# Kernel optimization log

Hardware: AMD Instinct MI355X
Metric: run time of the kernel (lower is better)

## Reference

```python
import jax, jax.numpy as jnp
import numpy as np

B, L, D = 4, 4096, 1024
DS, EXP, DC = 16, 2, 4
DI = EXP * D
K_SYM = max(3, 2 * DC + 1)  # 9


def _linear(x, w, b):
    # torch nn.Linear: y = x @ W^T + b, W:[out,in]
    return jnp.einsum('blc,oc->blo', x, w) + b


def _dwconv(x, kernel, bias, pad_l, pad_r):
    # x:[B,L,C], kernel:[C,1,k] depthwise, torch 'same' padding (asymmetric for even k)
    y = jax.lax.conv_general_dilated(
        x.transpose(0, 2, 1), kernel, window_strides=(1,),
        padding=[(pad_l, pad_r)], dimension_numbers=('NCH', 'OIH', 'NCH'),
        feature_group_count=x.shape[-1])
    return y.transpose(0, 2, 1) + bias


def _rmsnorm(x, w, eps=1e-6):
    scale = jax.lax.rsqrt(jnp.mean(x * x, axis=-1, keepdims=True) + eps)
    return w * x * scale


def setup_inputs() -> dict:
    key = jax.random.key(0)
    ks = jax.random.split(key, 12)
    def n(k, shape, s=0.02):
        return jax.random.normal(k, shape, jnp.float32) * s
    return {
        'x': jax.random.normal(ks[0], (B, L, D), jnp.float32),
        'norm_w': jnp.ones((D,), jnp.float32),
        'in_w': n(ks[1], (2 * DI, D)), 'in_b': jnp.zeros((2 * DI,), jnp.float32),
        'dwa_k': n(ks[2], (DI, 1, DC)), 'dwa_b': jnp.zeros((DI,), jnp.float32),
        'A': n(ks[3], (DI, DS)), 'Bm': n(ks[4], (DS, DI)),
        'sym_k': n(ks[5], (DI, 1, K_SYM)), 'sym_b': jnp.zeros((DI,), jnp.float32),
        'pw_w': n(ks[6], (DI, DI)), 'pw_b': jnp.zeros((DI,), jnp.float32),
        'ha_w': n(ks[7], (DI // 2, DI)), 'ha_b': jnp.zeros((DI // 2,), jnp.float32),
        'hb_w': n(ks[8], (DI // 2, DI)), 'hb_b': jnp.zeros((DI // 2,), jnp.float32),
        'fuse_w': n(ks[9], (DI, DI)), 'fuse_b': jnp.zeros((DI,), jnp.float32),
        'out_w': n(ks[10], (D, DI)), 'out_b': jnp.zeros((D,), jnp.float32),
    }


def reference(x, norm_w, in_w, in_b, dwa_k, dwa_b, A, Bm, sym_k, sym_b,
              pw_w, pw_b, ha_w, ha_b, hb_w, hb_b, fuse_w, fuse_b, out_w, out_b):
    residual = x
    h = _rmsnorm(x, norm_w)
    h = _linear(h, in_w, in_b)                       # [B,L,2*DI]
    gate, val = h[..., :DI], h[..., DI:]
    gate = jax.nn.sigmoid(gate)
    # mamba-like branch: depthwise conv (k=4, torch 'same' -> pad (1,2)) + low-rank A@B
    a = _dwconv(val, dwa_k, dwa_b, 1, 2)             # [B,L,DI]
    a = jnp.einsum('bld,ds->bls', a, A)              # [B,L,DS]
    a = jnp.einsum('bls,sd->bld', a, Bm)             # [B,L,DI]
    # symmetric conv branch: depthwise conv (k=9, pad (4,4)) -> silu -> pointwise linear
    b = _dwconv(val, sym_k, sym_b, K_SYM // 2, K_SYM // 2)
    b = jax.nn.silu(b)
    b = _linear(b, pw_w, pw_b)
    a = _linear(a, ha_w, ha_b)                       # [B,L,DI/2]
    b = _linear(b, hb_w, hb_b)                       # [B,L,DI/2]
    y = jnp.concatenate([a, b], axis=-1)             # [B,L,DI]
    y = _linear(y, fuse_w, fuse_b)
    y = gate * y
    y = _linear(y, out_w, out_b)                     # [B,L,D]
    return residual + y
```

## Files before the change

### kernel.cpp

```cpp
#include <hip/hip_runtime.h>
#include <hip/hip_bf16.h>
#include <stdint.h>

typedef __bf16 bf16;
typedef __bf16 bf16x8 __attribute__((ext_vector_type(8)));
typedef __bf16 bf16x4 __attribute__((ext_vector_type(4)));
typedef float  f32x4  __attribute__((ext_vector_type(4)));

#define LDS_PTR(p) ((__attribute__((address_space(3))) uint32_t*)(p))
#define GLB_PTR(p) ((const __attribute__((address_space(1))) uint32_t*)(p))

static constexpr int BATCH = 4, SEQ = 4096, DMODEL = 1024;
static constexpr int DI = 2048;
static constexpr int MTOK = BATCH * SEQ;

enum { EPI_SPLIT = 0, EPI_PLAIN = 1, EPI_GATE = 2, EPI_RES = 3, EPI_F32S = 4 };

template <int EPI, bool SPLITK = false, bool KEXT = false>
__global__ __launch_bounds__(256) void gemm_bt(
    const bf16* __restrict__ Aact, const bf16* __restrict__ W,
    const float* __restrict__ bias,
    bf16* __restrict__ out0, bf16* __restrict__ out1,
    const bf16* __restrict__ gate,
    float* __restrict__ outf, const float* __restrict__ resid,
    int N, int K, int ldC, int col_off,
    const bf16* __restrict__ Ax, const bf16* __restrict__ Bx)
{
  __shared__ __align__(16) bf16 sA[128 * 64];
  __shared__ __align__(16) bf16 sB[128 * 64];
  const int tid  = threadIdx.x;
  int n0, m0, kbeg, kend;
  size_t out_off = 0;
  if (SPLITK) {
    n0 = blockIdx.z * 128;
    m0 = blockIdx.y * 128;
    const int kh = K / gridDim.x;
    kbeg = blockIdx.x * kh; kend = kbeg + kh;
    out_off = (EPI == EPI_F32S) ? (size_t)blockIdx.x * (size_t)col_off
                                : (size_t)blockIdx.x * ((size_t)MTOK * 128);
  } else {
    const int nT  = gridDim.x;
    const int lin = blockIdx.y * nT + blockIdx.x;
    const int grp = lin / (8 * nT);
    const int within = lin - grp * (8 * nT);
    n0 = (within >> 3) * 128;
    m0 = (grp * 8 + (within & 7)) * 128;
    kbeg = 0; kend = K;
  }
  const int lane = tid & 63;
  const int wv   = tid >> 6;
  const int wr   = wv >> 1, wc = wv & 1;
  const int l15  = lane & 15, quad = lane >> 4;

  f32x4 acc[4][4];
#pragma unroll
  for (int i = 0; i < 4; ++i)
#pragma unroll
    for (int j = 0; j < 4; ++j) acc[i][j] = (f32x4){0.f, 0.f, 0.f, 0.f};

  int rr[4], cb[4];
#pragma unroll
  for (int j = 0; j < 4; ++j) {
    const int s = tid + j * 256;
    rr[j] = s >> 3;
    cb[j] = ((s & 7) ^ (rr[j] & 7)) * 16;
  }

  const char* gA = (const char*)(Aact + (size_t)m0 * K);
  const char* gW = (const char*)(W + (size_t)n0 * K);

  const int ntile = (kend - kbeg) >> 6;
  const int ttot  = KEXT ? ntile + 1 : ntile;
  for (int ti = 0; ti < ttot; ++ti) {
    if (ti) __syncthreads();
    if (!KEXT || ti < ntile) {
      const int k0 = kbeg + ti * 64;
#pragma unroll
      for (int j = 0; j < 4; ++j)
        __builtin_amdgcn_global_load_lds(GLB_PTR(gA + ((size_t)rr[j] * K + k0) * 2 + cb[j]),
                                         LDS_PTR(sA + (tid + j * 256) * 8), 16, 0, 0);
#pragma unroll
      for (int j = 0; j < 4; ++j)
        __builtin_amdgcn_global_load_lds(GLB_PTR(gW + ((size_t)rr[j] * K + k0) * 2 + cb[j]),
                                         LDS_PTR(sB + (tid + j * 256) * 8), 16, 0, 0);
    } else {
#pragma unroll
      for (int j = 0; j < 4; ++j)
        __builtin_amdgcn_global_load_lds(GLB_PTR((const char*)Ax + ((size_t)(m0 + rr[j]) * 64) * 2 + cb[j]),
                                         LDS_PTR(sA + (tid + j * 256) * 8), 16, 0, 0);
#pragma unroll
      for (int j = 0; j < 4; ++j)
        __builtin_amdgcn_global_load_lds(GLB_PTR((const char*)Bx + ((size_t)(n0 + rr[j]) * 64) * 2 + cb[j]),
                                         LDS_PTR(sB + (tid + j * 256) * 8), 16, 0, 0);
    }
    __syncthreads();

#pragma unroll
    for (int h = 0; h < 2; ++h) {
      bf16x8 av[4], bv[4];
#pragma unroll
      for (int t = 0; t < 4; ++t) {
        const int Ra = wr * 64 + t * 16 + l15;
        const int Rb = wc * 64 + t * 16 + l15;
        const int cc = h * 4 + quad;
        av[t] = *(const bf16x8*)(sA + (Ra * 8 + (cc ^ (Ra & 7))) * 8);
        bv[t] = *(const bf16x8*)(sB + (Rb * 8 + (cc ^ (Rb & 7))) * 8);
      }
#pragma unroll
      for (int i = 0; i < 4; ++i)
#pragma unroll
        for (int j = 0; j < 4; ++j)
          acc[i][j] = __builtin_amdgcn_mfma_f32_16x16x32_bf16(av[i], bv[j], acc[i][j], 0, 0, 0);
    }
  }

  bf16*  o0 = out0 + out_off;
  float* of = outf ? outf + out_off : nullptr;
#pragma unroll
  for (int i = 0; i < 4; ++i) {
    const int mbase = m0 + wr * 64 + i * 16 + quad * 4;
#pragma unroll
    for (int j = 0; j < 4; ++j) {
      const int n = n0 + wc * 64 + j * 16 + l15;
      const float bj = bias ? bias[n] : 0.f;
#pragma unroll
      for (int r = 0; r < 4; ++r) {
        const int mm = mbase + r;
        float v = acc[i][j][r] + bj;
        if (EPI == EPI_SPLIT) {
          if (n < DI) o0[(size_t)mm * DI + n] = (bf16)(1.f / (1.f + __expf(-v)));
          else        out1[(size_t)mm * DI + (n - DI)] = (bf16)v;
        } else if (EPI == EPI_PLAIN) {
          o0[(size_t)mm * ldC + col_off + n] = (bf16)v;
        } else if (EPI == EPI_GATE) {
          const float g = (float)gate[(size_t)mm * DI + n];
          o0[(size_t)mm * ldC + n] = (bf16)(v * g);
        } else if (EPI == EPI_F32S) {
          of[(size_t)mm * ldC + n] = v;
        } else {
          outf[(size_t)mm * ldC + n] = v + resid[(size_t)mm * ldC + n];
        }
      }
    }
  }
}

__global__ __launch_bounds__(256) void rmsnorm_kernel(
    const float* __restrict__ x, const float* __restrict__ w, bf16* __restrict__ out)
{
  const int row = blockIdx.x;
  const int tid = threadIdx.x;
  const float4 xv = ((const float4*)(x + (size_t)row * DMODEL))[tid];
  float s = xv.x * xv.x + xv.y * xv.y + xv.z * xv.z + xv.w * xv.w;
#pragma unroll
  for (int o = 32; o; o >>= 1) s += __shfl_xor(s, o);
  __shared__ float red[4];
  if ((tid & 63) == 0) red[tid >> 6] = s;
  __syncthreads();
  const float tot = red[0] + red[1] + red[2] + red[3];
  const float scale = rsqrtf(tot * (1.f / DMODEL) + 1e-6f);
  const float4 wv = ((const float4*)w)[tid];
  bf16x4 o4 = { (bf16)(xv.x * wv.x * scale), (bf16)(xv.y * wv.y * scale),
                (bf16)(xv.z * wv.z * scale), (bf16)(xv.w * wv.w * scale) };
  *(bf16x4*)(out + (size_t)row * DMODEL + tid * 4) = o4;
}

static constexpr int TL2 = 32;
__global__ __launch_bounds__(256) void conv_kernel(
    const bf16* __restrict__ val,
    const float* __restrict__ sym_k, const float* __restrict__ sym_b,
    bf16* __restrict__ bbuf)
{
  const int d  = (blockIdx.y * 256 + threadIdx.x) * 4;
  const int b  = blockIdx.z;
  const int l0 = blockIdx.x * TL2;
  float wk[9][4], bs[4];
#pragma unroll
  for (int j = 0; j < 4; ++j) {
    bs[j] = sym_b[d + j];
#pragma unroll
    for (int k = 0; k < 9; ++k) wk[k][j] = sym_k[(d + j) * 9 + k];
  }
  const bf16* base = val + (size_t)b * SEQ * DI + d;

  float win[9][4];
#pragma unroll
  for (int j = 0; j < 8; ++j) {
    const int xr = l0 + j - 4;
    if (xr >= 0 && xr < SEQ) {
      bf16x4 v = *(const bf16x4*)(base + (size_t)xr * DI);
#pragma unroll
      for (int c = 0; c < 4; ++c) win[j][c] = (float)v[c];
    } else {
#pragma unroll
      for (int c = 0; c < 4; ++c) win[j][c] = 0.f;
    }
  }
  for (int t = 0; t < TL2; ++t) {
    const int xf = l0 + t + 4;
    if (xf < SEQ) {
      bf16x4 v = *(const bf16x4*)(base + (size_t)xf * DI);
#pragma unroll
      for (int c = 0; c < 4; ++c) win[8][c] = (float)v[c];
    } else {
#pragma unroll
      for (int c = 0; c < 4; ++c) win[8][c] = 0.f;
    }
    float sb[4];
#pragma unroll
    for (int c = 0; c < 4; ++c) sb[c] = bs[c];
#pragma unroll
    for (int k = 0; k < 9; ++k)
#pragma unroll
      for (int c = 0; c < 4; ++c) sb[c] += win[k][c] * wk[k][c];
    bf16x4 o;
#pragma unroll
    for (int c = 0; c < 4; ++c) o[c] = (bf16)(sb[c] / (1.f + __expf(-sb[c])));
    *(bf16x4*)(bbuf + ((size_t)b * SEQ + l0 + t) * DI + d) = o;
#pragma unroll
    for (int k = 0; k < 8; ++k)
#pragma unroll
      for (int c = 0; c < 4; ++c) win[k][c] = win[k + 1][c];
  }
}

__global__ __launch_bounds__(256) void prep_cvt_kernel(
    const float* __restrict__ in_w, const float* __restrict__ hb_w,
    const float* __restrict__ out_w, const float* __restrict__ pw_w,
    bf16* __restrict__ in_wbf, bf16* __restrict__ hb_bf,
    bf16* __restrict__ out_bf, bf16* __restrict__ pwT_bf)
{
  __shared__ float s[32][33];
  const int b = blockIdx.x;
  const int tid = threadIdx.x;
  if (b < 8192) {
    const float* src; bf16* dst; size_t i;
    if (b < 4096)      { src = in_w;  dst = in_wbf; i = (size_t)b * 256 + tid; }
    else if (b < 6144) { src = hb_w;  dst = hb_bf;  i = (size_t)(b - 4096) * 256 + tid; }
    else               { src = out_w; dst = out_bf; i = (size_t)(b - 6144) * 256 + tid; }
    const float4 v = ((const float4*)src)[i];
    bf16x4 o4 = { (bf16)v.x, (bf16)v.y, (bf16)v.z, (bf16)v.w };
    *(bf16x4*)(dst + 4 * i) = o4;
  } else {
    const int q = b - 8192;
    const int d0 = (q & 63) * 32, c0 = (q >> 6) * 32;
    const int r = tid >> 5, x = tid & 31;
#pragma unroll
    for (int rr = r; rr < 32; rr += 8)
      s[rr][x] = pw_w[(size_t)(c0 + rr) * 2048 + d0 + x];
    __syncthreads();
#pragma unroll
    for (int rr = r; rr < 32; rr += 8)
      pwT_bf[(size_t)(d0 + rr) * 2048 + c0 + x] = (bf16)s[x][rr];
  }
}

__global__ __launch_bounds__(256) void prep_small_kernel(
    const float* __restrict__ Bm, const float* __restrict__ ha_w,
    const float* __restrict__ dwa_b, const float* __restrict__ dwa_k,
    const float* __restrict__ A,
    const float* __restrict__ hb_w, const float* __restrict__ pw_b,
    const float* __restrict__ hb_b, const float* __restrict__ fuse_w,
    const float* __restrict__ Hp,
    float* __restrict__ T1, float* __restrict__ cvec, float* __restrict__ b_H,
    bf16* __restrict__ Wp, bf16* __restrict__ Fb, bf16* __restrict__ Ht)
{
  const int b = blockIdx.x, tid = threadIdx.x;
  __shared__ float red[4][16];
  if (b < 1024) {
    const int o = b;
    float acc[16];
#pragma unroll
    for (int s = 0; s < 16; ++s) acc[s] = 0.f;
    for (int d = tid; d < 2048; d += 256) {
      const float w = ha_w[(size_t)o * 2048 + d];
#pragma unroll
      for (int s = 0; s < 16; ++s) acc[s] += Bm[s * 2048 + d] * w;
    }
    const int lane = tid & 63, wv = tid >> 6;
#pragma unroll
    for (int s = 0; s < 16; ++s) {
      float v = acc[s];
#pragma unroll
      for (int off = 32; off; off >>= 1) v += __shfl_xor(v, off);
      if (lane == s) red[wv][s] = v;
    }
    __syncthreads();
    if (tid < 16)
      T1[tid * 1024 + o] = red[0][tid] + red[1][tid] + red[2][tid] + red[3][tid];
  } else if (b == 1024) {
    float acc[16];
#pragma unroll
    for (int s = 0; s < 16; ++s) acc[s] = 0.f;
    for (int d = tid; d < 2048; d += 256) {
      const float w = dwa_b[d];
#pragma unroll
      for (int s = 0; s < 16; ++s) acc[s] += w * A[d * 16 + s];
    }
    const int lane = tid & 63, wv = tid >> 6;
#pragma unroll
    for (int s = 0; s < 16; ++s) {
      float v = acc[s];
#pragma unroll
      for (int off = 32; off; off >>= 1) v += __shfl_xor(v, off);
      if (lane == s) red[wv][s] = v;
    }
    __syncthreads();
    if (tid < 16) cvec[tid] = red[0][tid] + red[1][tid] + red[2][tid] + red[3][tid];
  } else if (b < 1029) {
    const int o = (b - 1025) * 256 + tid;
    float acc = hb_b[o];
    const float* hr = hb_w + (size_t)o * 2048;
    for (int c = 0; c < 2048; c += 4) {
      float4 h = *(const float4*)(hr + c);
      float4 p = *(const float4*)(pw_b + c);
      acc += h.x * p.x + h.y * p.y + h.z * p.z + h.w * p.w;
    }
    b_H[o] = acc;
  } else if (b < 1037) {
    const int d = (b - 1029) * 256 + tid;
    float kk[4], av[16];
#pragma unroll
    for (int k = 0; k < 4; ++k) kk[k] = dwa_k[d * 4 + k];
#pragma unroll
    for (int s = 0; s < 16; ++s) av[s] = A[d * 16 + s];
#pragma unroll
    for (int k = 0; k < 4; ++k)
#pragma unroll
      for (int s = 0; s < 16; ++s)
        Wp[(size_t)(k * 16 + s) * 2048 + d] = (bf16)(kk[k] * av[s]);
    for (int n = 64; n < 128; ++n) Wp[(size_t)n * 2048 + d] = (bf16)0.f;
  } else if (b < 3085) {
    const int idx = (b - 1037) * 256 + tid;
    const int n = idx >> 8, o4 = idx & 255;
    float4 v = ((const float4*)(fuse_w + (size_t)n * 2048 + 1024))[o4];
    bf16x4 o = { (bf16)v.x, (bf16)v.y, (bf16)v.z, (bf16)v.w };
    *(bf16x4*)(Fb + (size_t)n * 1024 + o4 * 4) = o;
  } else {
    const size_t e4 = (size_t)(b - 3085) * 256 + tid;
    float4 p0 = ((const float4*)Hp)[e4];
    float4 p1 = ((const float4*)(Hp + 2048 * 1024))[e4];
    bf16x4 o = { (bf16)(p0.x + p1.x), (bf16)(p0.y + p1.y),
                 (bf16)(p0.z + p1.z), (bf16)(p0.w + p1.w) };
    *(bf16x4*)(Ht + e4 * 4) = o;
  }
}

__global__ __launch_bounds__(256) void prep_fuse_kernel(
    const float* __restrict__ T1, const float* __restrict__ fuse_w,
    const float* __restrict__ fuse_b, const float* __restrict__ ha_b,
    const float* __restrict__ b_H,
    bf16* __restrict__ T2e, float* __restrict__ bias_z)
{
  const int b = blockIdx.x, tid = threadIdx.x;
  if (b < 128) {
    const int n = b * 16 + (tid >> 4);
    const int s = tid & 15;
    const float* fr = fuse_w + (size_t)n * 2048;
    const float* tr = T1 + s * 1024;
    float acc = 0.f;
    for (int o = 0; o < 1024; o += 4) {
      float4 f = *(const float4*)(fr + o);
      float4 t = *(const float4*)(tr + o);
      acc += f.x * t.x + f.y * t.y + f.z * t.z + f.w * t.w;
    }
    T2e[(size_t)n * 64 + s]      = (bf16)acc;
    T2e[(size_t)n * 64 + s + 16] = (bf16)0.f;
    T2e[(size_t)n * 64 + s + 32] = (bf16)0.f;
    T2e[(size_t)n * 64 + s + 48] = (bf16)0.f;
  } else {
    const int n = b - 128;
    const float* fr = fuse_w + (size_t)n * 2048;
    const int o = tid * 4;
    float4 fa = *(const float4*)(fr + o);
    float4 fb = *(const float4*)(fr + 1024 + o);
    float4 ha = *(const float4*)(ha_b + o);
    float4 bh = *(const float4*)(b_H + o);
    float acc = fa.x * ha.x + fa.y * ha.y + fa.z * ha.z + fa.w * ha.w
              + fb.x * bh.x + fb.y * bh.y + fb.z * bh.z + fb.w * bh.w;
#pragma unroll
    for (int off = 32; off; off >>= 1) acc += __shfl_xor(acc, off);
    __shared__ float r4[4];
    if ((tid & 63) == 0) r4[tid >> 6] = acc;
    __syncthreads();
    if (tid == 0) bias_z[n] = fuse_b[n] + r4[0] + r4[1] + r4[2] + r4[3];
  }
}

__global__ __launch_bounds__(256) void s16_kernel(
    const bf16* __restrict__ P0, const bf16* __restrict__ P1,
    const float* __restrict__ cvec, bf16* __restrict__ s16e)
{
  const int g = blockIdx.x * 256 + threadIdx.x;
  const int tok = g >> 4, s = g & 15;
  const int l = tok & (SEQ - 1), bb = tok >> 12;
  float acc = cvec[s];
#pragma unroll
  for (int k = 0; k < 4; ++k) {
    const int r = l - 1 + k;
    if ((unsigned)r < (unsigned)SEQ) {
      const size_t idx = ((size_t)bb * SEQ + r) * 128 + k * 16 + s;
      acc += (float)P0[idx] + (float)P1[idx];
    }
  }
  s16e[(size_t)tok * 64 + s]      = (bf16)acc;
  s16e[(size_t)tok * 64 + s + 16] = (bf16)0.f;
  s16e[(size_t)tok * 64 + s + 32] = (bf16)0.f;
  s16e[(size_t)tok * 64 + s + 48] = (bf16)0.f;
}

extern "C" void kernel_launch(void* const* d_in, const int* in_sizes, int n_in,
                              void* d_out, int out_size, void* d_ws, size_t ws_size,
                              hipStream_t stream)
{
  const float* x      = (const float*)d_in[0];
  const float* norm_w = (const float*)d_in[1];
  const float* in_w   = (const float*)d_in[2];
  const float* in_b   = (const float*)d_in[3];
  const float* dwa_k  = (const float*)d_in[4];
  const float* dwa_b  = (const float*)d_in[5];
  const float* Amat   = (const float*)d_in[6];
  const float* Bm     = (const float*)d_in[7];
  const float* sym_k  = (const float*)d_in[8];
  const float* sym_b  = (const float*)d_in[9];
  const float* pw_w   = (const float*)d_in[10];
  const float* pw_b   = (const float*)d_in[11];
  const float* ha_w   = (const float*)d_in[12];
  const float* ha_b   = (const float*)d_in[13];
  const float* hb_w   = (const float*)d_in[14];
  const float* hb_b   = (const float*)d_in[15];
  const float* fuse_w = (const float*)d_in[16];
  const float* fuse_b = (const float*)d_in[17];
  const float* out_w  = (const float*)d_in[18];
  const float* out_b  = (const float*)d_in[19];
  float* out = (float*)d_out;

  char* ws = (char*)d_ws;
  const size_t MB = 1u << 20, KB = 1u << 10;
  bf16*  in_wbf  = (bf16*)(ws + 0);
  bf16*  hnorm   = (bf16*)(ws + 8 * MB);
  bf16*  bsilu   = (bf16*)(ws + 0);
  float* Hpart   = (float*)(ws + 64 * MB);
  bf16*  valp    = (bf16*)(ws + 64 * MB);
  bf16*  zbuf    = (bf16*)(ws + 64 * MB);
  bf16*  gatep   = (bf16*)(ws + 128 * MB);
  bf16*  Pbuf    = (bf16*)(ws + 192 * MB);
  bf16*  pwT_bf  = (bf16*)(ws + 200 * MB);
  bf16*  WB_bf   = (bf16*)(ws + 200 * MB);
  bf16*  hb_bf   = (bf16*)(ws + 208 * MB);
  bf16*  Fb_bf   = (bf16*)(ws + 208 * MB);
  bf16*  s16e    = (bf16*)(ws + 208 * MB);
  bf16*  Ht_bf   = (bf16*)(ws + 212 * MB);
  bf16*  out_bf  = (bf16*)(ws + 216 * MB);
  float* T1      = (float*)(ws + 220 * MB);
  float* cvec    = (float*)(ws + 220 * MB + 64 * KB);
  float* b_H     = (float*)(ws + 220 * MB + 68 * KB);
  float* bias_z  = (float*)(ws + 220 * MB + 72 * KB);
  bf16*  Wp      = (bf16*)(ws + 220 * MB + 80 * KB);
  bf16*  T2e     = (bf16*)(ws + 220 * MB + 592 * KB);

  prep_cvt_kernel<<<12288, 256, 0, stream>>>(
      in_w, hb_w, out_w, pw_w, in_wbf, hb_bf, out_bf, pwT_bf);
  gemm_bt<EPI_F32S, true><<<dim3(2, 16, 8), 256, 0, stream>>>(
      pwT_bf, hb_bf, nullptr, nullptr, nullptr, nullptr, Hpart, nullptr,
      1024, 2048, 1024, 2048 * 1024, nullptr, nullptr);
  prep_small_kernel<<<5133, 256, 0, stream>>>(
      Bm, ha_w, dwa_b, dwa_k, Amat, hb_w, pw_b, hb_b, fuse_w, Hpart,
      T1, cvec, b_H, Wp, Fb_bf, Ht_bf);
  gemm_bt<EPI_PLAIN><<<dim3(16, 16), 256, 0, stream>>>(
      Fb_bf, Ht_bf, nullptr, WB_bf, nullptr, nullptr, nullptr, nullptr,
      2048, 1024, 2048, 0, nullptr, nullptr);
  prep_fuse_kernel<<<2176, 256, 0, stream>>>(T1, fuse_w, fuse_b, ha_b, b_H, T2e, bias_z);

  rmsnorm_kernel<<<MTOK, 256, 0, stream>>>(x, norm_w, hnorm);
  gemm_bt<EPI_SPLIT><<<dim3(32, 128), 256, 0, stream>>>(
      hnorm, in_wbf, in_b, gatep, valp, nullptr, nullptr, nullptr,
      4096, 1024, DI, 0, nullptr, nullptr);
  conv_kernel<<<dim3(SEQ / TL2, 2, BATCH), 256, 0, stream>>>(
      valp, sym_k, sym_b, bsilu);
  gemm_bt<EPI_PLAIN, true><<<dim3(2, 128), 256, 0, stream>>>(
      valp, Wp, nullptr, Pbuf, nullptr, nullptr, nullptr, nullptr,
      128, 2048, 128, 0, nullptr, nullptr);
  s16_kernel<<<MTOK * 16 / 256, 256, 0, stream>>>(
      Pbuf, Pbuf + (size_t)MTOK * 128, cvec, s16e);
  gemm_bt<EPI_GATE, false, true><<<dim3(16, 128), 256, 0, stream>>>(
      bsilu, WB_bf, bias_z, zbuf, nullptr, gatep, nullptr, nullptr,
      2048, 2048, 2048, 0, s16e, T2e);
  gemm_bt<EPI_RES><<<dim3(8, 128), 256, 0, stream>>>(
      zbuf, out_bf, out_b, nullptr, nullptr, nullptr, out, x,
      1024, 2048, 1024, 0, nullptr, nullptr);
}
```

Measured before the change: 836.7 us.

## Restructure weight-prep pipeline with wider split-K and merged prep kernels

Merges the small precompute work into the first conversion kernel so it runs concurrently with the bf16 weight casts. The Ht split-K GEMM grid is widened (8 K-partitions reduced by a new combine kernel), and the WB GEMM becomes split-K with fp32 partials reduced inside prep_fuse. The T2e dot products are spread over four threads each with shuffle reductions. The aim is to fill the GPU during the small weight-preprocessing GEMMs, at the cost of extra fp32 partial traffic and one added launch.

Result: faster. 806.3 us (-3.6%).

```diff
diff --git a/kernel.cpp b/kernel.cpp
--- a/kernel.cpp
+++ b/kernel.cpp
@@ -224,15 +224,21 @@
   }
 }
 
-__global__ __launch_bounds__(256) void prep_cvt_kernel(
+__global__ __launch_bounds__(256) void prep1_kernel(
     const float* __restrict__ in_w, const float* __restrict__ hb_w,
     const float* __restrict__ out_w, const float* __restrict__ pw_w,
+    const float* __restrict__ Bm, const float* __restrict__ ha_w,
+    const float* __restrict__ dwa_b, const float* __restrict__ dwa_k,
+    const float* __restrict__ A, const float* __restrict__ pw_b,
+    const float* __restrict__ hb_b, const float* __restrict__ fuse_w,
     bf16* __restrict__ in_wbf, bf16* __restrict__ hb_bf,
-    bf16* __restrict__ out_bf, bf16* __restrict__ pwT_bf)
+    bf16* __restrict__ out_bf, bf16* __restrict__ pwT_bf,
+    float* __restrict__ T1, float* __restrict__ cvec, float* __restrict__ b_H,
+    bf16* __restrict__ Wp, bf16* __restrict__ Fb)
 {
   __shared__ float s[32][33];
-  const int b = blockIdx.x;
-  const int tid = threadIdx.x;
+  __shared__ float red[4][16];
+  const int b = blockIdx.x, tid = threadIdx.x;
   if (b < 8192) {
     const float* src; bf16* dst; size_t i;
     if (b < 4096)      { src = in_w;  dst = in_wbf; i = (size_t)b * 256 + tid; }
@@ -241,7 +247,7 @@
     const float4 v = ((const float4*)src)[i];
     bf16x4 o4 = { (bf16)v.x, (bf16)v.y, (bf16)v.z, (bf16)v.w };
     *(bf16x4*)(dst + 4 * i) = o4;
-  } else {
+  } else if (b < 12288) {
     const int q = b - 8192;
     const int d0 = (q & 63) * 32, c0 = (q >> 6) * 32;
     const int r = tid >> 5, x = tid & 31;
@@ -252,63 +258,48 @@
 #pragma unroll
     for (int rr = r; rr < 32; rr += 8)
       pwT_bf[(size_t)(d0 + rr) * 2048 + c0 + x] = (bf16)s[x][rr];
-  }
-}
-
-__global__ __launch_bounds__(256) void prep_small_kernel(
-    const float* __restrict__ Bm, const float* __restrict__ ha_w,
-    const float* __restrict__ dwa_b, const float* __restrict__ dwa_k,
-    const float* __restrict__ A,
-    const float* __restrict__ hb_w, const float* __restrict__ pw_b,
-    const float* __restrict__ hb_b, const float* __restrict__ fuse_w,
-    const float* __restrict__ Hp,
-    float* __restrict__ T1, float* __restrict__ cvec, float* __restrict__ b_H,
-    bf16* __restrict__ Wp, bf16* __restrict__ Fb, bf16* __restrict__ Ht)
-{
-  const int b = blockIdx.x, tid = threadIdx.x;
-  __shared__ float red[4][16];
-  if (b < 1024) {
-    const int o = b;
+  } else if (b < 13312) {
+    const int o = b - 12288;
     float acc[16];
 #pragma unroll
-    for (int s = 0; s < 16; ++s) acc[s] = 0.f;
+    for (int ss = 0; ss < 16; ++ss) acc[ss] = 0.f;
     for (int d = tid; d < 2048; d += 256) {
       const float w = ha_w[(size_t)o * 2048 + d];
 #pragma unroll
-      for (int s = 0; s < 16; ++s) acc[s] += Bm[s * 2048 + d] * w;
+      for (int ss = 0; ss < 16; ++ss) acc[ss] += Bm[ss * 2048 + d] * w;
     }
     const int lane = tid & 63, wv = tid >> 6;
 #pragma unroll
-    for (int s = 0; s < 16; ++s) {
-      float v = acc[s];
+    for (int ss = 0; ss < 16; ++ss) {
+      float v = acc[ss];
 #pragma unroll
       for (int off = 32; off; off >>= 1) v += __shfl_xor(v, off);
-      if (lane == s) red[wv][s] = v;
+      if (lane == ss) red[wv][ss] = v;
     }
     __syncthreads();
     if (tid < 16)
       T1[tid * 1024 + o] = red[0][tid] + red[1][tid] + red[2][tid] + red[3][tid];
-  } else if (b == 1024) {
+  } else if (b == 13312) {
     float acc[16];
 #pragma unroll
-    for (int s = 0; s < 16; ++s) acc[s] = 0.f;
+    for (int ss = 0; ss < 16; ++ss) acc[ss] = 0.f;
     for (int d = tid; d < 2048; d += 256) {
       const float w = dwa_b[d];
 #pragma unroll
-      for (int s = 0; s < 16; ++s) acc[s] += w * A[d * 16 + s];
+      for (int ss = 0; ss < 16; ++ss) acc[ss] += w * A[d * 16 + ss];
     }
     const int lane = tid & 63, wv = tid >> 6;
 #pragma unroll
-    for (int s = 0; s < 16; ++s) {
-      float v = acc[s];
+    for (int ss = 0; ss < 16; ++ss) {
+      float v = acc[ss];
 #pragma unroll
       for (int off = 32; off; off >>= 1) v += __shfl_xor(v, off);
-      if (lane == s) red[wv][s] = v;
+      if (lane == ss) red[wv][ss] = v;
     }
     __syncthreads();
     if (tid < 16) cvec[tid] = red[0][tid] + red[1][tid] + red[2][tid] + red[3][tid];
-  } else if (b < 1029) {
-    const int o = (b - 1025) * 256 + tid;
+  } else if (b < 13317) {
+    const int o = (b - 13313) * 256 + tid;
     float acc = hb_b[o];
     const float* hr = hb_w + (size_t)o * 2048;
     for (int c = 0; c < 2048; c += 4) {
@@ -317,59 +308,71 @@
       acc += h.x * p.x + h.y * p.y + h.z * p.z + h.w * p.w;
     }
     b_H[o] = acc;
-  } else if (b < 1037) {
-    const int d = (b - 1029) * 256 + tid;
+  } else if (b < 13325) {
+    const int d = (b - 13317) * 256 + tid;
     float kk[4], av[16];
 #pragma unroll
     for (int k = 0; k < 4; ++k) kk[k] = dwa_k[d * 4 + k];
 #pragma unroll
-    for (int s = 0; s < 16; ++s) av[s] = A[d * 16 + s];
+    for (int ss = 0; ss < 16; ++ss) av[ss] = A[d * 16 + ss];
 #pragma unroll
     for (int k = 0; k < 4; ++k)
 #pragma unroll
-      for (int s = 0; s < 16; ++s)
-        Wp[(size_t)(k * 16 + s) * 2048 + d] = (bf16)(kk[k] * av[s]);
+      for (int ss = 0; ss < 16; ++ss)
+        Wp[(size_t)(k * 16 + ss) * 2048 + d] = (bf16)(kk[k] * av[ss]);
     for (int n = 64; n < 128; ++n) Wp[(size_t)n * 2048 + d] = (bf16)0.f;
-  } else if (b < 3085) {
-    const int idx = (b - 1037) * 256 + tid;
+  } else {
+    const int idx = (b - 13325) * 256 + tid;
     const int n = idx >> 8, o4 = idx & 255;
     float4 v = ((const float4*)(fuse_w + (size_t)n * 2048 + 1024))[o4];
     bf16x4 o = { (bf16)v.x, (bf16)v.y, (bf16)v.z, (bf16)v.w };
     *(bf16x4*)(Fb + (size_t)n * 1024 + o4 * 4) = o;
-  } else {
-    const size_t e4 = (size_t)(b - 3085) * 256 + tid;
-    float4 p0 = ((const float4*)Hp)[e4];
-    float4 p1 = ((const float4*)(Hp + 2048 * 1024))[e4];
-    bf16x4 o = { (bf16)(p0.x + p1.x), (bf16)(p0.y + p1.y),
-                 (bf16)(p0.z + p1.z), (bf16)(p0.w + p1.w) };
-    *(bf16x4*)(Ht + e4 * 4) = o;
-  }
+  }
+}
+
+__global__ __launch_bounds__(256) void htcomb_kernel(
+    const float* __restrict__ Hp, bf16* __restrict__ Ht)
+{
+  const size_t e4 = (size_t)blockIdx.x * 256 + threadIdx.x;
+  float4 a = ((const float4*)Hp)[e4];
+#pragma unroll
+  for (int k = 1; k < 8; ++k) {
+    float4 p = ((const float4*)(Hp + (size_t)k * 2048 * 1024))[e4];
+    a.x += p.x; a.y += p.y; a.z += p.z; a.w += p.w;
+  }
+  bf16x4 o = { (bf16)a.x, (bf16)a.y, (bf16)a.z, (bf16)a.w };
+  *(bf16x4*)(Ht + e4 * 4) = o;
 }
 
 __global__ __launch_bounds__(256) void prep_fuse_kernel(
     const float* __restrict__ T1, const float* __restrict__ fuse_w,
     const float* __restrict__ fuse_b, const float* __restrict__ ha_b,
-    const float* __restrict__ b_H,
-    bf16* __restrict__ T2e, float* __restrict__ bias_z)
+    const float* __restrict__ b_H, const float* __restrict__ WBp,
+    bf16* __restrict__ T2e, float* __restrict__ bias_z, bf16* __restrict__ WB)
 {
   const int b = blockIdx.x, tid = threadIdx.x;
-  if (b < 128) {
-    const int n = b * 16 + (tid >> 4);
-    const int s = tid & 15;
+  if (b < 512) {
+    const int n = b * 4 + (tid >> 6);
+    const int s = (tid >> 2) & 15;
+    const int sub = tid & 3;
     const float* fr = fuse_w + (size_t)n * 2048;
     const float* tr = T1 + s * 1024;
     float acc = 0.f;
-    for (int o = 0; o < 1024; o += 4) {
+    for (int o = sub * 4; o < 1024; o += 16) {
       float4 f = *(const float4*)(fr + o);
       float4 t = *(const float4*)(tr + o);
       acc += f.x * t.x + f.y * t.y + f.z * t.z + f.w * t.w;
     }
-    T2e[(size_t)n * 64 + s]      = (bf16)acc;
-    T2e[(size_t)n * 64 + s + 16] = (bf16)0.f;
-    T2e[(size_t)n * 64 + s + 32] = (bf16)0.f;
-    T2e[(size_t)n * 64 + s + 48] = (bf16)0.f;
-  } else {
-    const int n = b - 128;
+    acc += __shfl_xor(acc, 1);
+    acc += __shfl_xor(acc, 2);
+    if (sub == 0) {
+      T2e[(size_t)n * 64 + s]      = (bf16)acc;
+      T2e[(size_t)n * 64 + s + 16] = (bf16)0.f;
+      T2e[(size_t)n * 64 + s + 32] = (bf16)0.f;
+      T2e[(size_t)n * 64 + s + 48] = (bf16)0.f;
+    }
+  } else if (b < 2560) {
+    const int n = b - 512;
     const float* fr = fuse_w + (size_t)n * 2048;
     const int o = tid * 4;
     float4 fa = *(const float4*)(fr + o);
@@ -384,6 +387,13 @@
     if ((tid & 63) == 0) r4[tid >> 6] = acc;
     __syncthreads();
     if (tid == 0) bias_z[n] = fuse_b[n] + r4[0] + r4[1] + r4[2] + r4[3];
+  } else {
+    const size_t e4 = (size_t)(b - 2560) * 256 + tid;
+    float4 p0 = ((const float4*)WBp)[e4];
+    float4 p1 = ((const float4*)(WBp + (size_t)2048 * 2048))[e4];
+    bf16x4 o = { (bf16)(p0.x + p1.x), (bf16)(p0.y + p1.y),
+                 (bf16)(p0.z + p1.z), (bf16)(p0.w + p1.w) };
+    *(bf16x4*)(WB + e4 * 4) = o;
   }
 }
 
@@ -441,6 +451,7 @@
   bf16*  hnorm   = (bf16*)(ws + 8 * MB);
   bf16*  bsilu   = (bf16*)(ws + 0);
   float* Hpart   = (float*)(ws + 64 * MB);
+  float* WBp     = (float*)(ws + 64 * MB);
   bf16*  valp    = (bf16*)(ws + 64 * MB);
   bf16*  zbuf    = (bf16*)(ws + 64 * MB);
   bf16*  gatep   = (bf16*)(ws + 128 * MB);
@@ -459,18 +470,18 @@
   bf16*  Wp      = (bf16*)(ws + 220 * MB + 80 * KB);
   bf16*  T2e     = (bf16*)(ws + 220 * MB + 592 * KB);
 
-  prep_cvt_kernel<<<12288, 256, 0, stream>>>(
-      in_w, hb_w, out_w, pw_w, in_wbf, hb_bf, out_bf, pwT_bf);
-  gemm_bt<EPI_F32S, true><<<dim3(2, 16, 8), 256, 0, stream>>>(
+  prep1_kernel<<<15373, 256, 0, stream>>>(
+      in_w, hb_w, out_w, pw_w, Bm, ha_w, dwa_b, dwa_k, Amat, pw_b, hb_b, fuse_w,
+      in_wbf, hb_bf, out_bf, pwT_bf, T1, cvec, b_H, Wp, Fb_bf);
+  gemm_bt<EPI_F32S, true><<<dim3(8, 16, 8), 256, 0, stream>>>(
       pwT_bf, hb_bf, nullptr, nullptr, nullptr, nullptr, Hpart, nullptr,
       1024, 2048, 1024, 2048 * 1024, nullptr, nullptr);
-  prep_small_kernel<<<5133, 256, 0, stream>>>(
-      Bm, ha_w, dwa_b, dwa_k, Amat, hb_w, pw_b, hb_b, fuse_w, Hpart,
-      T1, cvec, b_H, Wp, Fb_bf, Ht_bf);
-  gemm_bt<EPI_PLAIN><<<dim3(16, 16), 256, 0, stream>>>(
-      Fb_bf, Ht_bf, nullptr, WB_bf, nullptr, nullptr, nullptr, nullptr,
-      2048, 1024, 2048, 0, nullptr, nullptr);
-  prep_fuse_kernel<<<2176, 256, 0, stream>>>(T1, fuse_w, fuse_b, ha_b, b_H, T2e, bias_z);
+  htcomb_kernel<<<2048, 256, 0, stream>>>(Hpart, Ht_bf);
+  gemm_bt<EPI_F32S, true><<<dim3(2, 16, 16), 256, 0, stream>>>(
+      Fb_bf, Ht_bf, nullptr, nullptr, nullptr, nullptr, WBp, nullptr,
+      2048, 1024, 2048, 2048 * 2048, nullptr, nullptr);
+  prep_fuse_kernel<<<6656, 256, 0, stream>>>(
+      T1, fuse_w, fuse_b, ha_b, b_H, WBp, T2e, bias_z, WB_bf);
 
   rmsnorm_kernel<<<MTOK, 256, 0, stream>>>(x, norm_w, hnorm);
   gemm_bt<EPI_SPLIT><<<dim3(32, 128), 256, 0, stream>>>(
```
